# Kernel tuning notes

Hardware: AMD Instinct MI355X
Metric: run time of the kernel (lower is better)

Reference implementation:

```python
import jax, jax.numpy as jnp
import numpy as np

B, L, D_MODEL, N_HEADS = 2, 2048, 1024, 16
RANK = max(N_HEADS, int(D_MODEL * 0.25))            # 256
RANK_PER_HEAD = RANK // N_HEADS                      # 16
HEAD_DIM = D_MODEL // N_HEADS                        # 64


def _rope_cos_sin(L, head_dim, dtype=jnp.float32):
    half = head_dim // 2
    theta = 1.0 / (10000.0 ** (jnp.arange(half, dtype=dtype) / half))
    angles = jnp.arange(L, dtype=dtype)[:, None] * theta[None, :]   # [L, half]
    return jnp.cos(angles), jnp.sin(angles)


def _apply_rope(x, cos, sin):
    # x: [B, L, H, D]; pairs (even, odd) rotated by per-position angle.
    B, L, H, D = x.shape
    xp = x.reshape(B, L, H, D // 2, 2)
    x0, x1 = xp[..., 0], xp[..., 1]
    c = cos[None, :, None, :]
    s = sin[None, :, None, :]
    r0 = x0 * c - x1 * s
    r1 = x0 * s + x1 * c
    return jnp.stack([r0, r1], axis=-1).reshape(B, L, H, D)


def setup_inputs() -> dict:
    key = jax.random.key(0)
    ks = jax.random.split(key, 7)
    x = jax.random.normal(ks[0], (B, L, D_MODEL), dtype=jnp.float32)
    mask = jax.random.randint(ks[1], (B, L), 0, 2, dtype=jnp.int32)
    scale = 0.02
    Wq = jax.random.normal(ks[2], (RANK, D_MODEL), dtype=jnp.float32) * scale
    Wk = jax.random.normal(ks[3], (RANK, D_MODEL), dtype=jnp.float32) * scale
    Wv = jax.random.normal(ks[4], (RANK, D_MODEL), dtype=jnp.float32) * scale
    xav_u = float(np.sqrt(6.0 / (HEAD_DIM + RANK_PER_HEAD)))
    U = jax.random.uniform(ks[5], (N_HEADS, HEAD_DIM, RANK_PER_HEAD), dtype=jnp.float32, minval=-xav_u, maxval=xav_u)
    V = jax.random.uniform(ks[6], (N_HEADS, RANK_PER_HEAD, HEAD_DIM), dtype=jnp.float32, minval=-xav_u, maxval=xav_u)
    return {"x": x, "Wq": Wq, "Wk": Wk, "Wv": Wv, "U": U, "V": V, "mask": mask}


def reference(x, Wq, Wk, Wv, U, V, mask):
    Bq, Lq, _ = x.shape
    H, HD, RH = U.shape
    q_low = (x @ Wq.T).reshape(Bq, Lq, H, RH)
    k_low = (x @ Wk.T).reshape(Bq, Lq, H, RH)
    v_low = (x @ Wv.T).reshape(Bq, Lq, H, RH)
    # up-project q/k to head_dim via shared U
    q = jnp.einsum('hdr,blhr->blhd', U, q_low)
    k = jnp.einsum('hdr,blhr->blhd', U, k_low)
    cos, sin = _rope_cos_sin(Lq, HD, x.dtype)
    q = _apply_rope(q, cos, sin)
    k = _apply_rope(k, cos, sin)
    attn = jnp.einsum('blhd,bmhd->bhlm', q, k) / jnp.sqrt(jnp.asarray(HD, x.dtype))
    key_mask = mask.astype(bool)[:, None, None, :]           # [B,1,1,M]
    attn = jnp.where(key_mask, attn, jnp.asarray(-jnp.inf, attn.dtype))
    attn = jax.nn.softmax(attn, axis=-1)
    out = jnp.einsum('bhlm,bmhr->blhr', attn, v_low)
    out = jnp.einsum('blhr,hrd->blhd', out, V)
    return out.reshape(Bq, Lq, H * HD)
```

## Files before the change

### kernel.cpp

```cpp
#include <hip/hip_runtime.h>
#include <hip/hip_bf16.h>

typedef unsigned short u16;
typedef unsigned int u32;
typedef __bf16 bf16x8 __attribute__((ext_vector_type(8)));
typedef float f32x4 __attribute__((ext_vector_type(4)));

#define NB 2
#define NL 2048
#define NDM 1024
#define NH 16
#define NHD 64
#define NRH 16
#define NCOL 2304

#define QSCL 0.18033688011112042f

#define AS1(p) ((const __attribute__((address_space(1))) void*)(p))
#define AS3(p) ((__attribute__((address_space(3))) void*)(p))

__device__ __forceinline__ u16 f2bf(float f) {
  u32 u = __builtin_bit_cast(u32, f);
  u32 r = (u + 0x7fffu + ((u >> 16) & 1u)) >> 16;
  return (u16)r;
}
__device__ __forceinline__ float bf2f(u16 b) {
  return __builtin_bit_cast(float, (u32)b << 16);
}

__global__ void k_prep_weff(const float* __restrict__ Wq, const float* __restrict__ Wk,
                            const float* __restrict__ Wv, const float* __restrict__ U,
                            u16* __restrict__ Wall) {
  int idx = blockIdx.x * 256 + threadIdx.x;
  int col = idx & 1023;
  int row = idx >> 10;
  float acc;
  if (row < 2048) {
    const float* W = (row < 1024) ? Wq : Wk;
    int rr = row & 1023;
    int h = rr >> 6, d = rr & 63;
    const float* Uh = U + (h * NHD + d) * NRH;
    const float* Wr = W + (size_t)(h * NRH) * NDM + col;
    acc = 0.f;
#pragma unroll
    for (int r = 0; r < 16; ++r) acc += Uh[r] * Wr[(size_t)r * NDM];
  } else {
    acc = Wv[(size_t)(row - 2048) * NDM + col];
  }
  Wall[idx] = f2bf(acc);
}

__global__ void k_cast_x(const float* __restrict__ x, u16* __restrict__ xb) {
  int i = blockIdx.x * 256 + threadIdx.x;
  float2 v = *(const float2*)(x + (size_t)i * 2);
  ushort2 o;
  o.x = f2bf(v.x);
  o.y = f2bf(v.y);
  *(ushort2*)(xb + (size_t)i * 2) = o;
}

__global__ void k_rope_tab(float* __restrict__ ctab, float* __restrict__ stab) {
  int i = blockIdx.x * 256 + threadIdx.x;
  if (i >= NL * 32) return;
  int l = i >> 5, j = i & 31;
  float theta = 1.0f / powf(10000.0f, (float)j * (1.0f / 32.0f));
  float ang = (float)l * theta;
  ctab[i] = cosf(ang);
  stab[i] = sinf(ang);
}

__global__ void k_fbias(const int* __restrict__ mask, float* __restrict__ fb) {
  int i = blockIdx.x * 256 + threadIdx.x;
  fb[i] = mask[i] ? 0.f : -1e30f;
}

__global__ __launch_bounds__(256) void k_gemm(const u16* __restrict__ A,
                                              const u16* __restrict__ Bm,
                                              u16* __restrict__ C) {
  __shared__ char lds[32768];
  const int tid = threadIdx.x;
  const int wave = tid >> 6, lane = tid & 63;
  const int bm = blockIdx.x, bn = blockIdx.y;
  const int wr = wave >> 1, wc = wave & 1;
  const char* Ag = (const char*)(A + (size_t)bm * 128 * NDM);
  const char* Bg = (const char*)(Bm + (size_t)bn * 128 * NDM);
  f32x4 acc[4][4] = {};
  for (int kt = 0; kt < 16; ++kt) {
    __syncthreads();
#pragma unroll
    for (int i = 0; i < 4; ++i) {
      int off = wave * 4096 + i * 1024 + lane * 16;
      int src = off ^ ((off >> 3) & 0x70);
      int ga = (src >> 7) * 2048 + kt * 128 + (src & 127);
      __builtin_amdgcn_global_load_lds(AS1(Ag + ga), AS3(lds + wave * 4096 + i * 1024), 16, 0, 0);
      __builtin_amdgcn_global_load_lds(AS1(Bg + ga), AS3(lds + 16384 + wave * 4096 + i * 1024), 16, 0, 0);
    }
    __syncthreads();
#pragma unroll
    for (int kk = 0; kk < 2; ++kk) {
      bf16x8 af[4], bfr[4];
#pragma unroll
      for (int m = 0; m < 4; ++m) {
        int row = wr * 64 + m * 16 + (lane & 15);
        int byte = row * 128 + kk * 64 + ((lane >> 4) << 4);
        af[m] = *(const bf16x8*)(lds + (byte ^ ((row & 7) << 4)));
      }
#pragma unroll
      for (int n = 0; n < 4; ++n) {
        int row = wc * 64 + n * 16 + (lane & 15);
        int byte = row * 128 + kk * 64 + ((lane >> 4) << 4);
        bfr[n] = *(const bf16x8*)(lds + 16384 + (byte ^ ((row & 7) << 4)));
      }
#pragma unroll
      for (int m = 0; m < 4; ++m)
#pragma unroll
        for (int n = 0; n < 4; ++n)
          acc[m][n] = __builtin_amdgcn_mfma_f32_16x16x32_bf16(af[m], bfr[n], acc[m][n], 0, 0, 0);
    }
  }
  const int r0 = bm * 128 + wr * 64, c0 = bn * 128 + wc * 64;
#pragma unroll
  for (int m = 0; m < 4; ++m)
#pragma unroll
    for (int n = 0; n < 4; ++n)
#pragma unroll
      for (int r = 0; r < 4; ++r) {
        int row = r0 + m * 16 + ((lane >> 4) << 2) + r;
        int col = c0 + n * 16 + (lane & 15);
        C[(size_t)row * NCOL + col] = f2bf(acc[m][n][r]);
      }
}

__global__ void k_rope(const u16* __restrict__ pre, const float* __restrict__ ctab,
                       const float* __restrict__ stab, u16* __restrict__ qt,
                       u16* __restrict__ kt) {
  int i = blockIdx.x * 256 + threadIdx.x;
  int j = i & 31, hh = (i >> 5) & 15, l = (i >> 9) & 2047, b = i >> 20;
  float c = ctab[l * 32 + j], s = stab[l * 32 + j];
  const u16* prow = pre + (size_t)(b * NL + l) * NCOL;
  size_t oidx = ((size_t)((b * NH + hh) * NL + l)) * 64 + 2 * j;
  u16 a0 = prow[hh * 64 + 2 * j], a1 = prow[hh * 64 + 2 * j + 1];
  float x0 = bf2f(a0), x1 = bf2f(a1);
  qt[oidx] = f2bf((x0 * c - x1 * s) * QSCL);
  qt[oidx + 1] = f2bf((x0 * s + x1 * c) * QSCL);
  u16 b0 = prow[1024 + hh * 64 + 2 * j], b1 = prow[1024 + hh * 64 + 2 * j + 1];
  x0 = bf2f(b0);
  x1 = bf2f(b1);
  kt[oidx] = f2bf(x0 * c - x1 * s);
  kt[oidx + 1] = f2bf(x0 * s + x1 * c);
}

__global__ void k_vt(const u16* __restrict__ pre, u16* __restrict__ vT) {
  __shared__ u16 s[64][16];
  int blk = blockIdx.x;
  int t = blk & 31, h = (blk >> 5) & 15, b = blk >> 9;
  int tid = threadIdx.x;
  {
    int l = tid >> 2, rq = (tid & 3) * 4;
    const u16* src = pre + (size_t)(b * NL + t * 64 + l) * NCOL + 2048 + h * NRH + rq;
    *(uint2*)&s[l][rq] = *(const uint2*)src;
  }
  __syncthreads();
  {
    int r = tid >> 4, pq = (tid & 15) * 4;
    int kb = ((pq >> 5) & 1) * 16 + ((pq >> 2) & 1) * 32 + ((pq >> 3) & 3) * 4;
    ushort4 o;
    o.x = s[kb + 0][r];
    o.y = s[kb + 1][r];
    o.z = s[kb + 2][r];
    o.w = s[kb + 3][r];
    *(ushort4*)(vT + ((size_t)((b * NH + h) * NRH + r)) * NL + t * 64 + pq) = o;
  }
}

__global__ __launch_bounds__(256) void k_attn(const u16* __restrict__ qt,
                                              const u16* __restrict__ ktp,
                                              const u16* __restrict__ vT,
                                              const float* __restrict__ fbias,
                                              float* __restrict__ Oattn) {
  __shared__ char lds[16384];
  const int tid = threadIdx.x, wave = tid >> 6, lane = tid & 63;
  int blk = (int)blockIdx.x;
  blk = (blk & 7) * 128 + (blk >> 3);
  const int qtile = blk & 31, h = (blk >> 5) & 15, b = blk >> 9;
  const size_t bh = (size_t)(b * NH + h);
  const u16* Q = qt + (bh * NL + (size_t)qtile * 64) * 64;
  const u16* K = ktp + bh * NL * 64;
  const u16* Vt = vT + bh * NRH * NL;
  const float* fbb = fbias + b * NL;

  const int g = lane >> 4, qi = lane & 15;
  const int swq = (qi & 7) << 4;

  const int qr = wave * 16 + qi;
  bf16x8 qf0 = *(const bf16x8*)(Q + qr * 64 + g * 8);
  bf16x8 qf1 = *(const bf16x8*)(Q + qr * 64 + 32 + g * 8);

  f32x4 o = {0.f, 0.f, 0.f, 0.f};
  float M = -1e30f, Ls = 0.f;

  const u16* Vrow = Vt + (size_t)qi * NL + g * 8;
  const float* fbg = fbb + g * 4;
  int koff[4][2];
#pragma unroll
  for (int n = 0; n < 4; ++n)
#pragma unroll
    for (int dc = 0; dc < 2; ++dc)
      koff[n][dc] = (((n * 16 + qi) * 128 + dc * 64 + g * 16) ^ swq);

#pragma unroll
  for (int i = 0; i < 2; ++i) {
    int off = wave * 2048 + i * 1024 + lane * 16;
    int src = off ^ ((off >> 3) & 0x70);
    __builtin_amdgcn_global_load_lds(AS1((const char*)K + src),
                                     AS3(lds + wave * 2048 + i * 1024), 16, 0, 0);
  }

  int cur = 0;
  for (int t = 0; t < 32; ++t) {
    __syncthreads();
    if (t < 31) {
      const char* Kg = (const char*)(K + (size_t)(t + 1) * 4096);
      char* Kn = lds + (cur ^ 1) * 8192;
#pragma unroll
      for (int i = 0; i < 2; ++i) {
        int off = wave * 2048 + i * 1024 + lane * 16;
        int src = off ^ ((off >> 3) & 0x70);
        __builtin_amdgcn_global_load_lds(AS1(Kg + src),
                                         AS3(Kn + wave * 2048 + i * 1024), 16, 0, 0);
      }
    }
    const char* Kcur = lds + cur * 8192;

    const float* fbt = fbg + t * 64;
    f32x4 fb0 = *(const f32x4*)(fbt);
    f32x4 fb1 = *(const f32x4*)(fbt + 16);
    f32x4 fb2 = *(const f32x4*)(fbt + 32);
    f32x4 fb3 = *(const f32x4*)(fbt + 48);
    const u16* Vtt = Vrow + t * 64;
    bf16x8 vf0 = *(const bf16x8*)(Vtt);
    bf16x8 vf1 = *(const bf16x8*)(Vtt + 32);

    f32x4 s0, s1, s2, s3;
#define QK(n, dst, fbv)                                                    \
  {                                                                        \
    bf16x8 k0 = *(const bf16x8*)(Kcur + koff[n][0]);                       \
    bf16x8 k1 = *(const bf16x8*)(Kcur + koff[n][1]);                       \
    f32x4 z = __builtin_amdgcn_mfma_f32_16x16x32_bf16(k0, qf0, fbv, 0, 0, 0); \
    dst = __builtin_amdgcn_mfma_f32_16x16x32_bf16(k1, qf1, z, 0, 0, 0);    \
  }
    QK(0, s0, fb0) QK(1, s1, fb1) QK(2, s2, fb2) QK(3, s3, fb3)
#undef QK

    float m0 = fmaxf(fmaxf(s0[0], s0[1]), fmaxf(s0[2], s0[3]));
    float m1 = fmaxf(fmaxf(s1[0], s1[1]), fmaxf(s1[2], s1[3]));
    float m2 = fmaxf(fmaxf(s2[0], s2[1]), fmaxf(s2[2], s2[3]));
    float m3 = fmaxf(fmaxf(s3[0], s3[1]), fmaxf(s3[2], s3[3]));
    float mt = fmaxf(fmaxf(m0, m1), fmaxf(m2, m3));
    mt = fmaxf(mt, __shfl_xor(mt, 16));
    mt = fmaxf(mt, __shfl_xor(mt, 32));

    if (__any(mt > M + 8.f)) {
      float Mn = fmaxf(M, mt);
      float e = __builtin_amdgcn_exp2f(M - Mn);
      M = Mn;
      Ls *= e;
#pragma unroll
      for (int i = 0; i < 4; ++i) o[i] *= __shfl(e, g * 4 + i);
    }

    float p00 = __builtin_amdgcn_exp2f(s0[0] - M), p01 = __builtin_amdgcn_exp2f(s0[1] - M);
    float p02 = __builtin_amdgcn_exp2f(s0[2] - M), p03 = __builtin_amdgcn_exp2f(s0[3] - M);
    float p10 = __builtin_amdgcn_exp2f(s1[0] - M), p11 = __builtin_amdgcn_exp2f(s1[1] - M);
    float p12 = __builtin_amdgcn_exp2f(s1[2] - M), p13 = __builtin_amdgcn_exp2f(s1[3] - M);
    float p20 = __builtin_amdgcn_exp2f(s2[0] - M), p21 = __builtin_amdgcn_exp2f(s2[1] - M);
    float p22 = __builtin_amdgcn_exp2f(s2[2] - M), p23 = __builtin_amdgcn_exp2f(s2[3] - M);
    float p30 = __builtin_amdgcn_exp2f(s3[0] - M), p31 = __builtin_amdgcn_exp2f(s3[1] - M);
    float p32 = __builtin_amdgcn_exp2f(s3[2] - M), p33 = __builtin_amdgcn_exp2f(s3[3] - M);
    float rs = (((p00 + p01) + (p02 + p03)) + ((p10 + p11) + (p12 + p13))) +
               (((p20 + p21) + (p22 + p23)) + ((p30 + p31) + (p32 + p33)));
    rs += __shfl_xor(rs, 16);
    rs += __shfl_xor(rs, 32);
    Ls += rs;

    bf16x8 pf0, pf1;
    pf0[0] = (__bf16)p00; pf0[1] = (__bf16)p01; pf0[2] = (__bf16)p02; pf0[3] = (__bf16)p03;
    pf0[4] = (__bf16)p20; pf0[5] = (__bf16)p21; pf0[6] = (__bf16)p22; pf0[7] = (__bf16)p23;
    pf1[0] = (__bf16)p10; pf1[1] = (__bf16)p11; pf1[2] = (__bf16)p12; pf1[3] = (__bf16)p13;
    pf1[4] = (__bf16)p30; pf1[5] = (__bf16)p31; pf1[6] = (__bf16)p32; pf1[7] = (__bf16)p33;

    o = __builtin_amdgcn_mfma_f32_16x16x32_bf16(pf0, vf0, o, 0, 0, 0);
    o = __builtin_amdgcn_mfma_f32_16x16x32_bf16(pf1, vf1, o, 0, 0, 0);
    cur ^= 1;
  }

  const size_t qrow0 = bh * NL + (size_t)qtile * 64 + wave * 16;
#pragma unroll
  for (int i = 0; i < 4; ++i) {
    float Li = __shfl(Ls, g * 4 + i);
    Oattn[(qrow0 + g * 4 + i) * NRH + qi] = o[i] / Li;
  }
}

__global__ void k_proj(const float* __restrict__ Oattn, const float* __restrict__ V,
                       float* __restrict__ out) {
  int bl = blockIdx.x;
  int b = bl >> 11, l = bl & 2047;
  __shared__ float sO[256];
  int tid = threadIdx.x;
  sO[tid] = Oattn[((size_t)(b * NH + (tid >> 4)) * NL + l) * NRH + (tid & 15)];
  __syncthreads();
#pragma unroll
  for (int p = 0; p < 4; ++p) {
    int h = (tid >> 6) + p * 4;
    int d = tid & 63;
    float acc = 0.f;
    const float* Vh = V + (size_t)(h * NRH) * NHD + d;
    const float* Oh = sO + h * NRH;
#pragma unroll
    for (int r = 0; r < 16; ++r) acc += Oh[r] * Vh[(size_t)r * NHD];
    out[(size_t)bl * NDM + h * NHD + d] = acc;
  }
}

extern "C" void kernel_launch(void* const* d_in, const int* in_sizes, int n_in,
                              void* d_out, int out_size, void* d_ws, size_t ws_size,
                              hipStream_t stream) {
  (void)in_sizes; (void)n_in; (void)out_size; (void)ws_size;
  const float* x  = (const float*)d_in[0];
  const float* Wq = (const float*)d_in[1];
  const float* Wk = (const float*)d_in[2];
  const float* Wv = (const float*)d_in[3];
  const float* U  = (const float*)d_in[4];
  const float* Vm = (const float*)d_in[5];
  const int* mask = (const int*)d_in[6];
  float* out = (float*)d_out;
  char* ws = (char*)d_ws;

  u16* Wall   = (u16*)(ws);
  u16* xb     = (u16*)(ws + 4718592);
  u16* pre    = (u16*)(ws + 13107200);
  u16* qt     = (u16*)(ws + 31981568);
  u16* ktb    = (u16*)(ws + 40370176);
  u16* vT     = (u16*)(ws + 48758784);
  float* ctab = (float*)(ws + 50855936);
  float* stab = (float*)(ws + 51118080);
  float* Oattn = (float*)(ws + 4718592);
  float* fbias = (float*)(ws + 8912896);

  k_prep_weff<<<dim3(9216), dim3(256), 0, stream>>>(Wq, Wk, Wv, U, Wall);
  k_cast_x<<<dim3(8192), dim3(256), 0, stream>>>(x, xb);
  k_rope_tab<<<dim3(256), dim3(256), 0, stream>>>(ctab, stab);
  k_gemm<<<dim3(32, 18), dim3(256), 0, stream>>>(xb, Wall, pre);
  k_fbias<<<dim3(16), dim3(256), 0, stream>>>(mask, fbias);
  k_rope<<<dim3(8192), dim3(256), 0, stream>>>(pre, ctab, stab, qt, ktb);
  k_vt<<<dim3(1024), dim3(256), 0, stream>>>(pre, vT);
  k_attn<<<dim3(1024), dim3(256), 0, stream>>>(qt, ktb, vT, fbias, Oattn);
  k_proj<<<dim3(4096), dim3(256), 0, stream>>>(Oattn, Vm, out);
}
```

Before: 126.4 us.

## Load K tiles directly from global memory instead of LDS double buffering

The attention kernel drops the shared-memory double-buffered K staging (global_load_lds plus per-iteration __syncthreads) and has each wave read its K fragments straight from global memory into registers, unrolling the loop by two. This removes the block-wide barriers and the LDS traffic, and lets waves run independently. In exchange, each of the four waves now fetches the same K tile separately, which relies on L1/L2 hits and adds global-load latency exposure.

```diff
diff --git a/kernel.cpp b/kernel.cpp
--- a/kernel.cpp
+++ b/kernel.cpp
@@ -178,7 +178,6 @@
                                               const u16* __restrict__ vT,
                                               const float* __restrict__ fbias,
                                               float* __restrict__ Oattn) {
-  __shared__ char lds[16384];
   const int tid = threadIdx.x, wave = tid >> 6, lane = tid & 63;
   int blk = (int)blockIdx.x;
   blk = (blk & 7) * 128 + (blk >> 3);
@@ -190,7 +189,6 @@
   const float* fbb = fbias + b * NL;
 
   const int g = lane >> 4, qi = lane & 15;
-  const int swq = (qi & 7) << 4;
 
   const int qr = wave * 16 + qi;
   bf16x8 qf0 = *(const bf16x8*)(Q + qr * 64 + g * 8);
@@ -199,39 +197,21 @@
   f32x4 o = {0.f, 0.f, 0.f, 0.f};
   float M = -1e30f, Ls = 0.f;
 
+  const u16* Krow = K + (size_t)qi * 64 + g * 8;
   const u16* Vrow = Vt + (size_t)qi * NL + g * 8;
   const float* fbg = fbb + g * 4;
-  int koff[4][2];
-#pragma unroll
-  for (int n = 0; n < 4; ++n)
-#pragma unroll
-    for (int dc = 0; dc < 2; ++dc)
-      koff[n][dc] = (((n * 16 + qi) * 128 + dc * 64 + g * 16) ^ swq);
-
-#pragma unroll
-  for (int i = 0; i < 2; ++i) {
-    int off = wave * 2048 + i * 1024 + lane * 16;
-    int src = off ^ ((off >> 3) & 0x70);
-    __builtin_amdgcn_global_load_lds(AS1((const char*)K + src),
-                                     AS3(lds + wave * 2048 + i * 1024), 16, 0, 0);
-  }
-
-  int cur = 0;
+
+#pragma unroll 2
   for (int t = 0; t < 32; ++t) {
-    __syncthreads();
-    if (t < 31) {
-      const char* Kg = (const char*)(K + (size_t)(t + 1) * 4096);
-      char* Kn = lds + (cur ^ 1) * 8192;
-#pragma unroll
-      for (int i = 0; i < 2; ++i) {
-        int off = wave * 2048 + i * 1024 + lane * 16;
-        int src = off ^ ((off >> 3) & 0x70);
-        __builtin_amdgcn_global_load_lds(AS1(Kg + src),
-                                         AS3(Kn + wave * 2048 + i * 1024), 16, 0, 0);
-      }
-    }
-    const char* Kcur = lds + cur * 8192;
-
+    const u16* Kt = Krow + t * 4096;
+    bf16x8 k00 = *(const bf16x8*)(Kt);
+    bf16x8 k01 = *(const bf16x8*)(Kt + 32);
+    bf16x8 k10 = *(const bf16x8*)(Kt + 1024);
+    bf16x8 k11 = *(const bf16x8*)(Kt + 1024 + 32);
+    bf16x8 k20 = *(const bf16x8*)(Kt + 2048);
+    bf16x8 k21 = *(const bf16x8*)(Kt + 2048 + 32);
+    bf16x8 k30 = *(const bf16x8*)(Kt + 3072);
+    bf16x8 k31 = *(const bf16x8*)(Kt + 3072 + 32);
     const float* fbt = fbg + t * 64;
     f32x4 fb0 = *(const f32x4*)(fbt);
     f32x4 fb1 = *(const f32x4*)(fbt + 16);
@@ -242,15 +222,14 @@
     bf16x8 vf1 = *(const bf16x8*)(Vtt + 32);
 
     f32x4 s0, s1, s2, s3;
-#define QK(n, dst, fbv)                                                    \
-  {                                                                        \
-    bf16x8 k0 = *(const bf16x8*)(Kcur + koff[n][0]);                       \
-    bf16x8 k1 = *(const bf16x8*)(Kcur + koff[n][1]);                       \
-    f32x4 z = __builtin_amdgcn_mfma_f32_16x16x32_bf16(k0, qf0, fbv, 0, 0, 0); \
-    dst = __builtin_amdgcn_mfma_f32_16x16x32_bf16(k1, qf1, z, 0, 0, 0);    \
-  }
-    QK(0, s0, fb0) QK(1, s1, fb1) QK(2, s2, fb2) QK(3, s3, fb3)
-#undef QK
+    s0 = __builtin_amdgcn_mfma_f32_16x16x32_bf16(k00, qf0, fb0, 0, 0, 0);
+    s0 = __builtin_amdgcn_mfma_f32_16x16x32_bf16(k01, qf1, s0, 0, 0, 0);
+    s1 = __builtin_amdgcn_mfma_f32_16x16x32_bf16(k10, qf0, fb1, 0, 0, 0);
+    s1 = __builtin_amdgcn_mfma_f32_16x16x32_bf16(k11, qf1, s1, 0, 0, 0);
+    s2 = __builtin_amdgcn_mfma_f32_16x16x32_bf16(k20, qf0, fb2, 0, 0, 0);
+    s2 = __builtin_amdgcn_mfma_f32_16x16x32_bf16(k21, qf1, s2, 0, 0, 0);
+    s3 = __builtin_amdgcn_mfma_f32_16x16x32_bf16(k30, qf0, fb3, 0, 0, 0);
+    s3 = __builtin_amdgcn_mfma_f32_16x16x32_bf16(k31, qf1, s3, 0, 0, 0);
 
     float m0 = fmaxf(fmaxf(s0[0], s0[1]), fmaxf(s0[2], s0[3]));
     float m1 = fmaxf(fmaxf(s1[0], s1[1]), fmaxf(s1[2], s1[3]));
@@ -291,7 +270,6 @@
 
     o = __builtin_amdgcn_mfma_f32_16x16x32_bf16(pf0, vf0, o, 0, 0, 0);
     o = __builtin_amdgcn_mfma_f32_16x16x32_bf16(pf1, vf1, o, 0, 0, 0);
-    cur ^= 1;
   }
 
   const size_t qrow0 = bh * NL + (size_t)qtile * 64 + wave * 16;
```

After: 229.9 us. +81.8%, slower.

## Fuse RoPE and V transpose into GEMM epilogue, drop intermediate buffer

Applied to the files above, without the earlier changes.

The projection GEMM now writes RoPE-rotated, scaled Q and K in head-major layout and the permuted transposed V directly from its accumulators. Adjacent even/odd columns are paired with a lane shuffle. This removes the separate rope and transpose kernels and the round trip through the 2304-column intermediate buffer. In exchange the GEMM epilogue gets more scattered 2-byte stores and per-element table loads, and the cos/sin tables are packed into a single float2 array.

```diff
diff --git a/kernel.cpp b/kernel.cpp
--- a/kernel.cpp
+++ b/kernel.cpp
@@ -23,9 +23,6 @@
   u32 u = __builtin_bit_cast(u32, f);
   u32 r = (u + 0x7fffu + ((u >> 16) & 1u)) >> 16;
   return (u16)r;
-}
-__device__ __forceinline__ float bf2f(u16 b) {
-  return __builtin_bit_cast(float, (u32)b << 16);
 }
 
 __global__ void k_prep_weff(const float* __restrict__ Wq, const float* __restrict__ Wk,
@@ -59,14 +56,13 @@
   *(ushort2*)(xb + (size_t)i * 2) = o;
 }
 
-__global__ void k_rope_tab(float* __restrict__ ctab, float* __restrict__ stab) {
+__global__ void k_cstab(float2* __restrict__ cstab) {
   int i = blockIdx.x * 256 + threadIdx.x;
   if (i >= NL * 32) return;
   int l = i >> 5, j = i & 31;
   float theta = 1.0f / powf(10000.0f, (float)j * (1.0f / 32.0f));
   float ang = (float)l * theta;
-  ctab[i] = cosf(ang);
-  stab[i] = sinf(ang);
+  cstab[i] = float2{cosf(ang), sinf(ang)};
 }
 
 __global__ void k_fbias(const int* __restrict__ mask, float* __restrict__ fb) {
@@ -76,7 +72,10 @@
 
 __global__ __launch_bounds__(256) void k_gemm(const u16* __restrict__ A,
                                               const u16* __restrict__ Bm,
-                                              u16* __restrict__ C) {
+                                              const float2* __restrict__ cstab,
+                                              u16* __restrict__ qt,
+                                              u16* __restrict__ ktb,
+                                              u16* __restrict__ vT) {
   __shared__ char lds[32768];
   const int tid = threadIdx.x;
   const int wave = tid >> 6, lane = tid & 63;
@@ -118,58 +117,55 @@
           acc[m][n] = __builtin_amdgcn_mfma_f32_16x16x32_bf16(af[m], bfr[n], acc[m][n], 0, 0, 0);
     }
   }
-  const int r0 = bm * 128 + wr * 64, c0 = bn * 128 + wc * 64;
-#pragma unroll
-  for (int m = 0; m < 4; ++m)
-#pragma unroll
-    for (int n = 0; n < 4; ++n)
-#pragma unroll
-      for (int r = 0; r < 4; ++r) {
-        int row = r0 + m * 16 + ((lane >> 4) << 2) + r;
-        int col = c0 + n * 16 + (lane & 15);
-        C[(size_t)row * NCOL + col] = f2bf(acc[m][n][r]);
-      }
-}
-
-__global__ void k_rope(const u16* __restrict__ pre, const float* __restrict__ ctab,
-                       const float* __restrict__ stab, u16* __restrict__ qt,
-                       u16* __restrict__ kt) {
-  int i = blockIdx.x * 256 + threadIdx.x;
-  int j = i & 31, hh = (i >> 5) & 15, l = (i >> 9) & 2047, b = i >> 20;
-  float c = ctab[l * 32 + j], s = stab[l * 32 + j];
-  const u16* prow = pre + (size_t)(b * NL + l) * NCOL;
-  size_t oidx = ((size_t)((b * NH + hh) * NL + l)) * 64 + 2 * j;
-  u16 a0 = prow[hh * 64 + 2 * j], a1 = prow[hh * 64 + 2 * j + 1];
-  float x0 = bf2f(a0), x1 = bf2f(a1);
-  qt[oidx] = f2bf((x0 * c - x1 * s) * QSCL);
-  qt[oidx + 1] = f2bf((x0 * s + x1 * c) * QSCL);
-  u16 b0 = prow[1024 + hh * 64 + 2 * j], b1 = prow[1024 + hh * 64 + 2 * j + 1];
-  x0 = bf2f(b0);
-  x1 = bf2f(b1);
-  kt[oidx] = f2bf(x0 * c - x1 * s);
-  kt[oidx + 1] = f2bf(x0 * s + x1 * c);
-}
-
-__global__ void k_vt(const u16* __restrict__ pre, u16* __restrict__ vT) {
-  __shared__ u16 s[64][16];
-  int blk = blockIdx.x;
-  int t = blk & 31, h = (blk >> 5) & 15, b = blk >> 9;
-  int tid = threadIdx.x;
-  {
-    int l = tid >> 2, rq = (tid & 3) * 4;
-    const u16* src = pre + (size_t)(b * NL + t * 64 + l) * NCOL + 2048 + h * NRH + rq;
-    *(uint2*)&s[l][rq] = *(const uint2*)src;
-  }
-  __syncthreads();
-  {
-    int r = tid >> 4, pq = (tid & 15) * 4;
-    int kb = ((pq >> 5) & 1) * 16 + ((pq >> 2) & 1) * 32 + ((pq >> 3) & 3) * 4;
-    ushort4 o;
-    o.x = s[kb + 0][r];
-    o.y = s[kb + 1][r];
-    o.z = s[kb + 2][r];
-    o.w = s[kb + 3][r];
-    *(ushort4*)(vT + ((size_t)((b * NH + h) * NRH + r)) * NL + t * 64 + pq) = o;
+
+  const int r0 = bm * 128 + wr * 64;
+  const int b = r0 >> 11;
+  if (bn < 16) {
+    const bool isq = (bn < 8);
+    u16* dst = isq ? qt : ktb;
+    const float qs = isq ? QSCL : 1.0f;
+    const int hh = (isq ? bn : bn - 8) * 2 + wc;
+    const int par = lane & 1;
+    const size_t base = ((size_t)(b * NH + hh)) * NL;
+#pragma unroll
+    for (int n = 0; n < 4; ++n) {
+      const int d = n * 16 + (lane & 15);
+      const int j = d >> 1;
+#pragma unroll
+      for (int m = 0; m < 4; ++m) {
+#pragma unroll
+        for (int r = 0; r < 4; ++r) {
+          int row = r0 + m * 16 + ((lane >> 4) << 2) + r;
+          int l = row & 2047;
+          float2 cs = cstab[l * 32 + j];
+          float v = acc[m][n][r];
+          float pv = __shfl_xor(v, 1);
+          float ov = par ? (pv * cs.y + v * cs.x) : (v * cs.x - pv * cs.y);
+          dst[((base + l) << 6) + d] = f2bf(ov * qs);
+        }
+      }
+    }
+  } else {
+    const int rr = lane & 15;
+#pragma unroll
+    for (int n = 0; n < 4; ++n) {
+      const int hh = (bn - 16) * 8 + wc * 4 + n;
+      const size_t vbase = ((size_t)(b * NH + hh) * NRH + rr) * NL;
+#pragma unroll
+      for (int m = 0; m < 4; ++m) {
+        int row0 = r0 + m * 16 + ((lane >> 4) << 2);
+        int l = row0 & 2047;
+        int l6 = l & 63;
+        int P = (l & ~63) | (((l6 >> 4) & 1) << 5) | (((l6 >> 5) & 1) << 2) |
+                (((l6 >> 2) & 3) << 3) | (l6 & 3);
+        ushort4 o4;
+        o4.x = f2bf(acc[m][n][0]);
+        o4.y = f2bf(acc[m][n][1]);
+        o4.z = f2bf(acc[m][n][2]);
+        o4.w = f2bf(acc[m][n][3]);
+        *(ushort4*)(vT + vbase + P) = o4;
+      }
+    }
   }
 }
 
@@ -337,24 +333,20 @@
   float* out = (float*)d_out;
   char* ws = (char*)d_ws;
 
-  u16* Wall   = (u16*)(ws);
-  u16* xb     = (u16*)(ws + 4718592);
-  u16* pre    = (u16*)(ws + 13107200);
-  u16* qt     = (u16*)(ws + 31981568);
-  u16* ktb    = (u16*)(ws + 40370176);
-  u16* vT     = (u16*)(ws + 48758784);
-  float* ctab = (float*)(ws + 50855936);
-  float* stab = (float*)(ws + 51118080);
-  float* Oattn = (float*)(ws + 4718592);
-  float* fbias = (float*)(ws + 8912896);
+  u16* Wall     = (u16*)(ws);
+  u16* xb       = (u16*)(ws + 4718592);
+  float* Oattn  = (float*)(ws + 13107200);
+  float* fbias  = (float*)(ws + 17301504);
+  u16* qt       = (u16*)(ws + 31981568);
+  u16* ktb      = (u16*)(ws + 40370176);
+  u16* vT       = (u16*)(ws + 48758784);
+  float2* cstab = (float2*)(ws + 50855936);
 
   k_prep_weff<<<dim3(9216), dim3(256), 0, stream>>>(Wq, Wk, Wv, U, Wall);
   k_cast_x<<<dim3(8192), dim3(256), 0, stream>>>(x, xb);
-  k_rope_tab<<<dim3(256), dim3(256), 0, stream>>>(ctab, stab);
-  k_gemm<<<dim3(32, 18), dim3(256), 0, stream>>>(xb, Wall, pre);
+  k_cstab<<<dim3(256), dim3(256), 0, stream>>>(cstab);
   k_fbias<<<dim3(16), dim3(256), 0, stream>>>(mask, fbias);
-  k_rope<<<dim3(8192), dim3(256), 0, stream>>>(pre, ctab, stab, qt, ktb);
-  k_vt<<<dim3(1024), dim3(256), 0, stream>>>(pre, vT);
+  k_gemm<<<dim3(32, 18), dim3(256), 0, stream>>>(xb, Wall, cstab, qt, ktb, vT);
   k_attn<<<dim3(1024), dim3(256), 0, stream>>>(qt, ktb, vT, fbias, Oattn);
   k_proj<<<dim3(4096), dim3(256), 0, stream>>>(Oattn, Vm, out);
 }
```

Measured after the change: 132.2 us. +4.6%, slower.
